# Kernel optimization log

Hardware: AMD Instinct MI355X
Metric: run time of the kernel (lower is better)

The kernel has to match this reference:

```python
import jax, jax.numpy as jnp
import numpy as np

T, B, V, E = 256, 128, 256, 512
NN = (1024, 1024)  # num_nodes per LSTM layer


def setup_inputs() -> dict:
    key = jax.random.key(0)
    ks = jax.random.split(key, 8)
    inputs = jax.random.normal(ks[0], (T, B, V), jnp.float32)
    emb = jax.random.normal(ks[1], (V, E), jnp.float32) * np.float32(np.sqrt(1.0 / V))
    w0 = jax.random.normal(ks[2], (E + NN[0], 4 * NN[0]), jnp.float32) * np.float32(np.sqrt(1.0 / (E + NN[0])))
    b0 = jnp.zeros((4 * NN[0],), jnp.float32)
    w1 = jax.random.normal(ks[3], (NN[0] + NN[1], 4 * NN[1]), jnp.float32) * np.float32(np.sqrt(1.0 / (NN[0] + NN[1])))
    b1 = jnp.zeros((4 * NN[1],), jnp.float32)
    out_w = jax.random.normal(ks[4], (NN[1], V), jnp.float32) * np.float32(np.sqrt(1.0 / NN[1]))
    out_b = jnp.zeros((V,), jnp.float32)
    return {"inputs": inputs, "embedding_matrix": emb,
            "lstm_w0": w0, "lstm_b0": b0, "lstm_w1": w1, "lstm_b1": b1,
            "out_w": out_w, "out_b": out_b}


def reference(inputs, embedding_matrix, lstm_w0, lstm_b0, lstm_w1, lstm_b1, out_w, out_b):
    Tn, Bn, _ = inputs.shape
    # _embed: (stacked one-hot) @ embedding_matrix -> [T, B, E]
    embs = jnp.einsum('tbv,ve->tbe', inputs, embedding_matrix)
    ws = (lstm_w0, lstm_w1)
    bs = (lstm_b0, lstm_b1)
    init_states = tuple((jnp.zeros((Bn, n), embs.dtype), jnp.zeros((Bn, n), embs.dtype)) for n in NN)

    def step(states, emb):
        out = emb
        new_states = []
        for i in range(len(NN)):
            h, c = states[i]
            n = NN[i]
            # concat([dropout(inp), h]) @ W + b ; dropout_keep_prob = 1.0 -> identity
            lin = jnp.concatenate([out, h], axis=1) @ ws[i] + bs[i]
            f = jax.nn.sigmoid(lin[:, :n])
            ig = jax.nn.sigmoid(lin[:, n:2 * n])
            o = jax.nn.sigmoid(lin[:, 2 * n:3 * n])
            g = jnp.tanh(lin[:, 3 * n:])
            c = f * c + ig * g
            h = o * jnp.tanh(c)
            out = h
            new_states.append((h, c))
        return tuple(new_states), out

    _, rnn_outputs = jax.lax.scan(step, init_states, embs)  # [T, B, NN[-1]]
    # output module: concat over time (axis 0) then single dense layer
    hs = rnn_outputs.reshape(Tn * Bn, NN[-1])
    logits = hs @ out_w + out_b  # [T*B, V]
    return logits
```

## Files before the change

### kernel.cpp

```cpp
#include <hip/hip_runtime.h>
#include <hip/hip_bf16.h>
#include <cstdint>
#include <cstddef>

#define T_STEPS 256
#define BATCH   128
#define VOCAB   256
#define EDIM    512
#define NH      1024
#define GDIM    4096
#define NST0    40
#define NST1    64

typedef __attribute__((ext_vector_type(8))) short short8;
typedef __attribute__((ext_vector_type(4))) float floatx4;

__device__ __forceinline__ float sigmoidf_(float x) { return 1.0f / (1.0f + __expf(-x)); }
__device__ __forceinline__ float tanhf_(float x)    { return 1.0f - 2.0f / (__expf(2.0f * x) + 1.0f); }

typedef __attribute__((address_space(1))) const unsigned int guint;
typedef __attribute__((address_space(3))) unsigned int luint;
__device__ __forceinline__ void load_lds16(const void* g, void* l) {
    __builtin_amdgcn_global_load_lds((guint*)g, (luint*)l, 16, 0, 0);
}

#define BM 128
#define BN 128
#define BK 16
__global__ __launch_bounds__(256) void sgemm_f32(
    const float* __restrict__ A, const float* __restrict__ B,
    float* __restrict__ C, int M, int N, int K)
{
    __shared__ float As[BK][BM + 4];
    __shared__ float Bs[BK][BN + 4];
    const int tid = threadIdx.x;
    const int tr = tid >> 4, tc = tid & 15;
    const int bm = blockIdx.y, bn = blockIdx.x;
    const float* Ab = A + (size_t)bm * BM * K;
    float acc[8][8];
    #pragma unroll
    for (int i = 0; i < 8; ++i)
        #pragma unroll
        for (int j = 0; j < 8; ++j) acc[i][j] = 0.f;
    for (int k0 = 0; k0 < K; k0 += BK) {
        #pragma unroll
        for (int l = 0; l < 2; ++l) {
            int idx = tid + l * 256;
            int row = idx >> 2, c4 = idx & 3;
            float4 v = *(const float4*)(Ab + (size_t)row * K + k0 + c4 * 4);
            As[c4 * 4 + 0][row] = v.x; As[c4 * 4 + 1][row] = v.y;
            As[c4 * 4 + 2][row] = v.z; As[c4 * 4 + 3][row] = v.w;
        }
        #pragma unroll
        for (int l = 0; l < 2; ++l) {
            int idx = tid + l * 256;
            int row = idx >> 5, c4 = idx & 31;
            *(float4*)&Bs[row][c4 * 4] = *(const float4*)(B + (size_t)(k0 + row) * N + bn * BN + c4 * 4);
        }
        __syncthreads();
        #pragma unroll
        for (int kk = 0; kk < BK; ++kk) {
            float4 a0 = *(const float4*)&As[kk][tr * 8];
            float4 a1 = *(const float4*)&As[kk][tr * 8 + 4];
            float4 b0 = *(const float4*)&Bs[kk][tc * 8];
            float4 b1 = *(const float4*)&Bs[kk][tc * 8 + 4];
            float av[8] = {a0.x, a0.y, a0.z, a0.w, a1.x, a1.y, a1.z, a1.w};
            float bv[8] = {b0.x, b0.y, b0.z, b0.w, b1.x, b1.y, b1.z, b1.w};
            #pragma unroll
            for (int i = 0; i < 8; ++i)
                #pragma unroll
                for (int j = 0; j < 8; ++j) acc[i][j] += av[i] * bv[j];
        }
        __syncthreads();
    }
    #pragma unroll
    for (int i = 0; i < 8; ++i) {
        size_t row = (size_t)bm * BM + tr * 8 + i;
        #pragma unroll
        for (int j = 0; j < 8; j += 4) {
            int col = bn * BN + tc * 8 + j;
            *(float4*)(C + row * N + col) =
                make_float4(acc[i][j], acc[i][j+1], acc[i][j+2], acc[i][j+3]);
        }
    }
}

__global__ __launch_bounds__(256) void transpose_to_bf16(
    const float* __restrict__ src, __hip_bfloat16* __restrict__ dst, int R, int C)
{
    __shared__ float t[32][33];
    int x = blockIdx.x * 32 + threadIdx.x;
    #pragma unroll
    for (int i = 0; i < 4; ++i) {
        int y = blockIdx.y * 32 + threadIdx.y + i * 8;
        t[threadIdx.y + i * 8][threadIdx.x] = src[(size_t)y * C + x];
    }
    __syncthreads();
    int x2 = blockIdx.y * 32 + threadIdx.x;
    #pragma unroll
    for (int i = 0; i < 4; ++i) {
        int y2 = blockIdx.x * 32 + threadIdx.y + i * 8;
        dst[(size_t)y2 * R + x2] = __float2bfloat16(t[threadIdx.x][threadIdx.y + i * 8]);
    }
}

__global__ __launch_bounds__(256) void pack_w2(
    const float* __restrict__ src, __hip_bfloat16* __restrict__ dst,
    int koff, int NSTEPS)
{
    __shared__ float t[64][33];
    const int tid = threadIdx.x;
    const int xt = blockIdx.x;
    const int kt = blockIdx.y;
    {
        int yl = tid >> 3;
        int x0 = (tid & 7) * 8;
        const float* p = src + (size_t)(kt * 32 + yl) * GDIM + xt * 64 + x0;
        float4 v0 = *(const float4*)p;
        float4 v1 = *(const float4*)(p + 4);
        t[x0 + 0][yl] = v0.x; t[x0 + 1][yl] = v0.y; t[x0 + 2][yl] = v0.z; t[x0 + 3][yl] = v0.w;
        t[x0 + 4][yl] = v1.x; t[x0 + 5][yl] = v1.y; t[x0 + 6][yl] = v1.z; t[x0 + 7][yl] = v1.w;
    }
    __syncthreads();
    {
        int ll = tid >> 2;
        int quad = tid & 3;
        int lincol = xt * 64 + ll;
        int g = lincol >> 10, n = lincol & 1023;
        int j = n >> 3, c = n & 7;
        int tt = g >> 1;
        int l16 = (g & 1) * 8 + c;
        int s = (koff >> 5) + kt;
        __hip_bfloat16 o[8];
        #pragma unroll
        for (int jj = 0; jj < 8; ++jj)
            o[jj] = __float2bfloat16(t[ll][quad * 8 + jj]);
        size_t off = ((((size_t)j * NSTEPS + s) * 2 + tt) * 64 + (size_t)quad * 16 + l16) * 8;
        *(uint4*)(dst + off) = *(const uint4*)o;
    }
}

__global__ __launch_bounds__(256) void convert_to_bf16(
    const float* __restrict__ src, __hip_bfloat16* __restrict__ dst, size_t n4)
{
    size_t i = (size_t)blockIdx.x * 256 + threadIdx.x;
    if (i < n4) {
        float4 v = *(const float4*)(src + i * 4);
        __hip_bfloat16 o[4] = {__float2bfloat16(v.x), __float2bfloat16(v.y),
                               __float2bfloat16(v.z), __float2bfloat16(v.w)};
        *(uint2*)(dst + i * 4) = *(uint2*)o;
    }
}

#define GKP 40
__global__ __launch_bounds__(256) void gemm_bt(
    const __hip_bfloat16* __restrict__ A, const __hip_bfloat16* __restrict__ Bt,
    const float* __restrict__ bias, float* __restrict__ C, int M, int N, int K)
{
    __shared__ __hip_bfloat16 As[128 * GKP];
    __shared__ __hip_bfloat16 Bs[128 * GKP];
    const int tid = threadIdx.x;
    const int wave = tid >> 6, lane = tid & 63;
    const int quad = lane >> 4, l16 = lane & 15;
    const int wm = (wave >> 1) * 64, wn = (wave & 1) * 64;
    const size_t Arow0 = (size_t)blockIdx.y * 128;
    const size_t Brow0 = (size_t)blockIdx.x * 128;
    floatx4 acc[4][4];
    #pragma unroll
    for (int i = 0; i < 4; ++i)
        #pragma unroll
        for (int j = 0; j < 4; ++j) acc[i][j] = (floatx4)0.f;

    for (int k0 = 0; k0 < K; k0 += 32) {
        #pragma unroll
        for (int l = 0; l < 2; ++l) {
            int idx = tid + l * 256;
            int row = idx >> 2, seg = idx & 3;
            *(uint4*)(As + row * GKP + seg * 8) =
                *(const uint4*)(A + (Arow0 + row) * K + k0 + seg * 8);
            *(uint4*)(Bs + row * GKP + seg * 8) =
                *(const uint4*)(Bt + (Brow0 + row) * K + k0 + seg * 8);
        }
        __syncthreads();
        short8 af[4], bf[4];
        #pragma unroll
        for (int i = 0; i < 4; ++i)
            af[i] = *(const short8*)(As + (wm + i * 16 + l16) * GKP + quad * 8);
        #pragma unroll
        for (int j = 0; j < 4; ++j)
            bf[j] = *(const short8*)(Bs + (wn + j * 16 + l16) * GKP + quad * 8);
        #pragma unroll
        for (int i = 0; i < 4; ++i)
            #pragma unroll
            for (int j = 0; j < 4; ++j)
                acc[i][j] = __builtin_amdgcn_mfma_f32_16x16x32_bf16(af[i], bf[j], acc[i][j], 0, 0, 0);
        __syncthreads();
    }
    #pragma unroll
    for (int i = 0; i < 4; ++i)
        #pragma unroll
        for (int j = 0; j < 4; ++j) {
            int col = (int)Brow0 + wn + j * 16 + l16;
            float bv = bias ? bias[col] : 0.f;
            #pragma unroll
            for (int r = 0; r < 4; ++r) {
                size_t row = Arow0 + wm + i * 16 + quad * 4 + r;
                C[row * N + col] = acc[i][j][r] + bv;
            }
        }
}

template<int NC, int W>
__device__ __forceinline__ void seg_run(
    const __hip_bfloat16* __restrict__ pA,
    const __hip_bfloat16* Wlds, int lane,
    floatx4& acc0, floatx4& acc1)
{
    constexpr int D = (NC < 3) ? NC : 3;
    short8 af[3][8];
    #pragma unroll
    for (int c = 0; c < D; ++c)
        #pragma unroll
        for (int ss = 0; ss < 8; ++ss)
            af[c][ss] = *(const short8*)(pA + (size_t)c * 256 + ss * 32);
    #pragma unroll
    for (int c = 0; c < NC; ++c) {
        #pragma unroll
        for (int ss = 0; ss < 8; ++ss) {
            const int s = (W + c) * 8 + ss;
            short8 bf0 = *(const short8*)&Wlds[s * 1024 + lane * 8];
            short8 bf1 = *(const short8*)&Wlds[s * 1024 + 512 + lane * 8];
            acc0 = __builtin_amdgcn_mfma_f32_16x16x32_bf16(af[c % 3][ss], bf0, acc0, 0, 0, 0);
            acc1 = __builtin_amdgcn_mfma_f32_16x16x32_bf16(af[c % 3][ss], bf1, acc1, 0, 0, 0);
        }
        if (c + 3 < NC) {
            #pragma unroll
            for (int ss = 0; ss < 8; ++ss)
                af[(c + 3) % 3][ss] = *(const short8*)(pA + (size_t)(c + 3) * 256 + ss * 32);
        }
    }
}

__global__ __launch_bounds__(512) void lstm_diag(
    const __hip_bfloat16* __restrict__ inbf,
    const __hip_bfloat16* __restrict__ Wpack0,
    const __hip_bfloat16* __restrict__ Wpack1,
    const float* __restrict__ b0, const float* __restrict__ b1,
    __hip_bfloat16* __restrict__ h0_cur,
    const __hip_bfloat16* __restrict__ h0_prev,
    float* __restrict__ c0, float* __restrict__ c1,
    __hip_bfloat16* __restrict__ H1all,
    int d)
{
    const int bid = blockIdx.x;
    const int layer = (bid >> 3) & 1;
    const int j = ((bid >> 4) << 3) | (bid & 7);
    if (layer == 0 && d >= T_STEPS) return;
    if (layer == 1 && d == 0) return;

    __shared__ __attribute__((aligned(16))) __hip_bfloat16 Wlds[65536];

    const int tid = threadIdx.x;
    const int wave = tid >> 6, lane = tid & 63;
    const int quad = lane >> 4, l16 = lane & 15;

    const __hip_bfloat16 *A0, *A1;
    int A0stride;
    const float* bb; float* cst; __hip_bfloat16* hout;
    bool first;
    if (layer == 0) {
        first = (d == 0);
        bb = b0; cst = c0;
        A0 = inbf + (size_t)d * (BATCH * VOCAB); A0stride = VOCAB;
        A1 = h0_prev;
        hout = h0_cur;
        const __hip_bfloat16* Wp = Wpack0 + (size_t)j * (NST0 * 1024);
        #pragma unroll
        for (int it = 0; it < 10; ++it)
            load_lds16(Wp + it * 4096 + tid * 8, Wlds + it * 4096 + tid * 8);
    } else {
        first = (d == 1);
        bb = b1; cst = c1;
        A0 = h0_prev; A0stride = NH;
        A1 = (d >= 2) ? (H1all + (size_t)(d - 2) * (BATCH * NH)) : h0_prev;
        hout = H1all + (size_t)(d - 1) * (BATCH * NH);
        const __hip_bfloat16* Wp = Wpack1 + (size_t)j * (NST1 * 1024);
        #pragma unroll
        for (int it = 0; it < 16; ++it)
            load_lds16(Wp + it * 4096 + tid * 8, Wlds + it * 4096 + tid * 8);
    }

    const int row = wave * 16 + l16;
    const __hip_bfloat16* pA0 = A0 + (size_t)row * A0stride + quad * 8;
    const __hip_bfloat16* pA1 = A1 + (size_t)row * NH + quad * 8;

    const int cc = j * 8 + (l16 & 7);
    float bv0 = bb[((l16 < 8) ? 0 : 1) * NH + cc];
    float bv1 = bb[((l16 < 8) ? 2 : 3) * NH + cc];
    float cold[4];
    {
        const int bbase = 16 * wave + quad * 4;
        #pragma unroll
        for (int r = 0; r < 4; ++r)
            cold[r] = first ? 0.f : cst[(size_t)(bbase + r) * NH + cc];
    }
    floatx4 acc0 = {bv0, bv0, bv0, bv0};
    floatx4 acc1 = {bv1, bv1, bv1, bv1};

    __syncthreads();
    if (layer == 0) {
        seg_run<1, 0>(pA0, Wlds, lane, acc0, acc1);
        if (!first) seg_run<4, 1>(pA1, Wlds, lane, acc0, acc1);
    } else {
        if (first) {
            seg_run<4, 0>(pA0, Wlds, lane, acc0, acc1);
        } else {
            seg_run<4, 4>(pA1, Wlds, lane, acc0, acc1);
            seg_run<4, 0>(pA0, Wlds, lane, acc0, acc1);
        }
    }

    #pragma unroll
    for (int r = 0; r < 4; ++r) {
        float a0 = acc0[r], a1 = acc1[r];
        float p0 = __shfl_xor(a0, 8, 64);
        float p1 = __shfl_xor(a1, 8, 64);
        if (l16 < 8) {
            int b = 16 * wave + quad * 4 + r;
            float f  = sigmoidf_(a0);
            float ig = sigmoidf_(p0);
            float oo = sigmoidf_(a1);
            float gg = tanhf_(p1);
            size_t idx = (size_t)b * NH + cc;
            float cn = f * cold[r] + ig * gg;
            float hn = oo * tanhf_(cn);
            cst[idx] = cn;
            hout[idx] = __float2bfloat16(hn);
        }
    }
}

__device__ __forceinline__ void spin_all_ge(const uint32_t* ep, uint32_t target,
                                            int lane, int wave) {
    asm volatile("" ::: "memory");
    if (wave == 0) {
        for (;;) {
            uint32_t a = __hip_atomic_load(&ep[lane], __ATOMIC_RELAXED, __HIP_MEMORY_SCOPE_AGENT);
            uint32_t b = __hip_atomic_load(&ep[lane + 64], __ATOMIC_RELAXED, __HIP_MEMORY_SCOPE_AGENT);
            if (__all(a >= target && b >= target)) break;
            __builtin_amdgcn_s_sleep(1);
        }
    }
    __builtin_amdgcn_s_barrier();
    asm volatile("" ::: "memory");
}

__device__ __forceinline__ void arrive_ep(uint32_t* slot, uint32_t val) {
    __syncthreads();
    asm volatile("" ::: "memory");
    if (threadIdx.x == 0)
        __hip_atomic_store(slot, val, __ATOMIC_RELAXED, __HIP_MEMORY_SCOPE_AGENT);
}

__global__ void zero_bar(uint32_t* p) { p[threadIdx.x] = 0; }

__device__ __forceinline__ void epilogue_store(
    floatx4 acc0, floatx4 acc1, float* creg, bool first,
    int wave, int quad, int l16, int cc8base,
    __hip_bfloat16* __restrict__ hout)
{
    #pragma unroll
    for (int r = 0; r < 4; ++r) {
        float a0 = acc0[r], a1 = acc1[r];
        float p0 = __shfl_xor(a0, 8, 64);
        float p1 = __shfl_xor(a1, 8, 64);
        float f  = sigmoidf_(a0);
        float ig = sigmoidf_(p0);
        float oo = sigmoidf_(a1);
        float gg = tanhf_(p1);
        float cn = f * (first ? 0.f : creg[r]) + ig * gg;
        if (l16 < 8) creg[r] = cn;
        float hn = oo * tanhf_(cn);
        union { __hip_bfloat16 h; unsigned short u; } cv;
        cv.h = __float2bfloat16(hn);
        unsigned int v1 = (unsigned int)cv.u |
                          (__shfl_xor((unsigned int)cv.u, 1, 64) << 16);
        unsigned int v2 = __shfl_xor(v1, 2, 64);
        unsigned long long p8 = (unsigned long long)v1 |
                                ((unsigned long long)v2 << 32);
        if (l16 == 0 || l16 == 4) {
            int b = 16 * wave + quad * 4 + r;
            __hip_atomic_store((unsigned long long*)&hout[(size_t)b * NH + cc8base + l16],
                               p8, __ATOMIC_RELAXED, __HIP_MEMORY_SCOPE_AGENT);
        }
    }
}

__global__ __launch_bounds__(512) void lstm_persist6(
    const __hip_bfloat16* __restrict__ inbf,
    const __hip_bfloat16* __restrict__ Wpack0,
    const __hip_bfloat16* __restrict__ Wpack1,
    const float* __restrict__ b0, const float* __restrict__ b1,
    __hip_bfloat16* __restrict__ H0all,
    __hip_bfloat16* __restrict__ H1all,
    uint32_t* __restrict__ bar)
{
    __shared__ __attribute__((aligned(16))) __hip_bfloat16 Wlds[65536];

    const int bid = blockIdx.x;
    const int layer = (bid >> 3) & 1;
    const int j = ((bid >> 4) << 3) | (bid & 7);
    const int tid = threadIdx.x;
    const int wave = tid >> 6, lane = tid & 63;
    const int quad = lane >> 4, l16 = lane & 15;

    uint32_t* ep0 = bar;
    uint32_t* ep1 = bar + 128;

    if (layer == 0) {
        const __hip_bfloat16* Wp = Wpack0 + (size_t)j * (NST0 * 1024);
        #pragma unroll
        for (int it = 0; it < 10; ++it)
            load_lds16(Wp + it * 4096 + tid * 8, Wlds + it * 4096 + tid * 8);
    } else {
        const __hip_bfloat16* Wp = Wpack1 + (size_t)j * (NST1 * 1024);
        #pragma unroll
        for (int it = 0; it < 16; ++it)
            load_lds16(Wp + it * 4096 + tid * 8, Wlds + it * 4096 + tid * 8);
    }
    __syncthreads();

    const int cc = j * 8 + (l16 & 7);
    const float* bb = layer ? b1 : b0;
    const float bv0 = bb[((l16 < 8) ? 0 : 1) * NH + cc];
    const float bv1 = bb[((l16 < 8) ? 2 : 3) * NH + cc];
    const int row = wave * 16 + l16;
    float creg[4] = {0.f, 0.f, 0.f, 0.f};

    if (layer == 0) {
        for (int d = 0; d < T_STEPS; ++d) {
            const bool first = (d == 0);
            const __hip_bfloat16* pX =
                inbf + (size_t)d * (BATCH * VOCAB) + (size_t)row * VOCAB + quad * 8;
            __hip_bfloat16* hout = H0all + (size_t)d * (BATCH * NH);
            floatx4 acc0 = {bv0, bv0, bv0, bv0};
            floatx4 acc1 = {bv1, bv1, bv1, bv1};
            seg_run<1, 0>(pX, Wlds, lane, acc0, acc1);
            if (!first) {
                spin_all_ge(ep0, (uint32_t)d, lane, wave);
                const __hip_bfloat16* pH0 =
                    H0all + (size_t)(d - 1) * (BATCH * NH) + (size_t)row * NH + quad * 8;
                seg_run<4, 1>(pH0, Wlds, lane, acc0, acc1);
            }
            epilogue_store(acc0, acc1, creg, first, wave, quad, l16, j * 8, hout);
            arrive_ep(&ep0[j], (uint32_t)(d + 1));
        }
    } else {
        for (int d = 1; d <= T_STEPS; ++d) {
            const bool first = (d == 1);
            __hip_bfloat16* hout = H1all + (size_t)(d - 1) * (BATCH * NH);
            floatx4 acc0 = {bv0, bv0, bv0, bv0};
            floatx4 acc1 = {bv1, bv1, bv1, bv1};
            if (!first) {
                spin_all_ge(ep1, (uint32_t)(d - 1), lane, wave);
                const __hip_bfloat16* pH1 =
                    H1all + (size_t)(d - 2) * (BATCH * NH) + (size_t)row * NH + quad * 8;
                seg_run<4, 4>(pH1, Wlds, lane, acc0, acc1);
            }
            spin_all_ge(ep0, (uint32_t)d, lane, wave);
            const __hip_bfloat16* pH0 =
                H0all + (size_t)(d - 1) * (BATCH * NH) + (size_t)row * NH + quad * 8;
            seg_run<4, 0>(pH0, Wlds, lane, acc0, acc1);
            epilogue_store(acc0, acc1, creg, first, wave, quad, l16, j * 8, hout);
            arrive_ep(&ep1[j], (uint32_t)d);
        }
    }
}

extern "C" void kernel_launch(void* const* d_in, const int* in_sizes, int n_in,
                              void* d_out, int out_size, void* d_ws, size_t ws_size,
                              hipStream_t stream)
{
    const float* inputs = (const float*)d_in[0];
    const float* emb    = (const float*)d_in[1];
    const float* w0     = (const float*)d_in[2];
    const float* b0     = (const float*)d_in[3];
    const float* w1     = (const float*)d_in[4];
    const float* b1     = (const float*)d_in[5];
    const float* outw   = (const float*)d_in[6];
    const float* outb   = (const float*)d_in[7];
    float* out = (float*)d_out;

    char* ws = (char*)d_ws;
    size_t off = 0;
    auto take = [&](size_t bytes) { char* p = ws + off; off += (bytes + 255) & ~(size_t)255; return p; };
    float* Wcomb = (float*)take((size_t)VOCAB * GDIM * 4);
    __hip_bfloat16* Wpack0 = (__hip_bfloat16*)take((size_t)128 * NST0 * 1024 * 2);
    __hip_bfloat16* Wpack1 = (__hip_bfloat16*)take((size_t)128 * NST1 * 1024 * 2);
    __hip_bfloat16* outwt  = (__hip_bfloat16*)take((size_t)NH * VOCAB * 2);
    __hip_bfloat16* inbf   = (__hip_bfloat16*)take((size_t)T_STEPS * BATCH * VOCAB * 2);
    __hip_bfloat16* h0pp0  = (__hip_bfloat16*)take((size_t)BATCH * NH * 2);
    __hip_bfloat16* h0pp1  = (__hip_bfloat16*)take((size_t)BATCH * NH * 2);
    float* c0 = (float*)take((size_t)BATCH * NH * 4);
    float* c1 = (float*)take((size_t)BATCH * NH * 4);
    uint32_t* bar = (uint32_t*)take(1024);
    __hip_bfloat16* H1all  = (__hip_bfloat16*)take((size_t)T_STEPS * BATCH * NH * 2);
    __hip_bfloat16* H0all  = (__hip_bfloat16*)take((size_t)T_STEPS * BATCH * NH * 2);
    const bool ws_ok = (off <= ws_size);

    sgemm_f32<<<dim3(GDIM / BN, VOCAB / BM), 256, 0, stream>>>(
        emb, w0, Wcomb, VOCAB, GDIM, EDIM);
    pack_w2<<<dim3(64, VOCAB / 32), 256, 0, stream>>>(Wcomb, Wpack0, 0, NST0);
    pack_w2<<<dim3(64, NH / 32), 256, 0, stream>>>(w0 + (size_t)EDIM * GDIM, Wpack0, VOCAB, NST0);
    pack_w2<<<dim3(64, NH / 32), 256, 0, stream>>>(w1, Wpack1, 0, NST1);
    pack_w2<<<dim3(64, NH / 32), 256, 0, stream>>>(w1 + (size_t)NH * GDIM, Wpack1, NH, NST1);
    transpose_to_bf16<<<dim3(VOCAB / 32, NH / 32), dim3(32, 8), 0, stream>>>(
        outw, outwt, NH, VOCAB);
    {
        size_t n4 = (size_t)T_STEPS * BATCH * VOCAB / 4;
        convert_to_bf16<<<(int)((n4 + 255) / 256), 256, 0, stream>>>(inputs, inbf, n4);
    }
    zero_bar<<<1, 256, 0, stream>>>(bar);

    bool done = false;
    if (ws_ok) {
        void* args[] = { (void*)&inbf, (void*)&Wpack0, (void*)&Wpack1,
                         (void*)&b0, (void*)&b1,
                         (void*)&H0all, (void*)&H1all, (void*)&bar };
        hipError_t ce = hipLaunchCooperativeKernel(lstm_persist6, dim3(256), dim3(512),
                                                   args, 0u, stream);
        done = (ce == hipSuccess);
    }
    if (!done) {
        for (int d = 0; d <= T_STEPS; ++d) {
            __hip_bfloat16* hcur = (d & 1) ? h0pp1 : h0pp0;
            __hip_bfloat16* hprev = (d & 1) ? h0pp0 : h0pp1;
            lstm_diag<<<256, 512, 0, stream>>>(
                inbf, Wpack0, Wpack1, b0, b1, hcur, hprev, c0, c1, H1all, d);
        }
    }

    gemm_bt<<<dim3(VOCAB / 128, (T_STEPS * BATCH) / 128), 256, 0, stream>>>(
        H1all, outwt, outb, out, T_STEPS * BATCH, VOCAB, NH);
}
```

Before: 4.793 ms.

## Hold LSTM weights in registers and split K across waves with LDS reduction

The persistent LSTM kernel no longer keeps its weight slice in LDS. Each wave now holds its share of the K dimension as MFMA B-fragments in registers, computes all 128 batch rows for that K-slice, and the per-wave partial sums are reduced through LDS before the gate epilogue. Every wave now spins on the barrier flags itself instead of wave 0 spinning and then calling s_barrier, and launch bounds ask for two blocks per CU. The aim is to remove repeated LDS weight reads and shorten the dependency chain per step. In exchange it adds an LDS reduction and a __syncthreads each step, and it puts heavy pressure on registers from the 8x2 accumulators plus the weight fragments.

```diff
diff --git a/kernel.cpp b/kernel.cpp
--- a/kernel.cpp
+++ b/kernel.cpp
@@ -340,18 +340,14 @@
     }
 }
 
-__device__ __forceinline__ void spin_all_ge(const uint32_t* ep, uint32_t target,
-                                            int lane, int wave) {
+__device__ __forceinline__ void spin_wave(const uint32_t* ep, uint32_t target, int lane) {
     asm volatile("" ::: "memory");
-    if (wave == 0) {
-        for (;;) {
-            uint32_t a = __hip_atomic_load(&ep[lane], __ATOMIC_RELAXED, __HIP_MEMORY_SCOPE_AGENT);
-            uint32_t b = __hip_atomic_load(&ep[lane + 64], __ATOMIC_RELAXED, __HIP_MEMORY_SCOPE_AGENT);
-            if (__all(a >= target && b >= target)) break;
-            __builtin_amdgcn_s_sleep(1);
-        }
-    }
-    __builtin_amdgcn_s_barrier();
+    for (;;) {
+        uint32_t a = __hip_atomic_load(&ep[lane], __ATOMIC_RELAXED, __HIP_MEMORY_SCOPE_AGENT);
+        uint32_t b = __hip_atomic_load(&ep[lane + 64], __ATOMIC_RELAXED, __HIP_MEMORY_SCOPE_AGENT);
+        if (__all(a >= target && b >= target)) break;
+        __builtin_amdgcn_s_sleep(1);
+    }
     asm volatile("" ::: "memory");
 }
 
@@ -396,7 +392,7 @@
     }
 }
 
-__global__ __launch_bounds__(512) void lstm_persist6(
+__global__ __launch_bounds__(512, 2) void lstm_persist7(
     const __hip_bfloat16* __restrict__ inbf,
     const __hip_bfloat16* __restrict__ Wpack0,
     const __hip_bfloat16* __restrict__ Wpack1,
@@ -405,75 +401,155 @@
     __hip_bfloat16* __restrict__ H1all,
     uint32_t* __restrict__ bar)
 {
-    __shared__ __attribute__((aligned(16))) __hip_bfloat16 Wlds[65536];
+    __shared__ __attribute__((aligned(16))) float red[32768];
 
     const int bid = blockIdx.x;
     const int layer = (bid >> 3) & 1;
     const int j = ((bid >> 4) << 3) | (bid & 7);
     const int tid = threadIdx.x;
-    const int wave = tid >> 6, lane = tid & 63;
+    const int wv = tid >> 6, lane = tid & 63;
     const int quad = lane >> 4, l16 = lane & 15;
 
     uint32_t* ep0 = bar;
     uint32_t* ep1 = bar + 128;
 
+    short8 breg[8][2];
     if (layer == 0) {
         const __hip_bfloat16* Wp = Wpack0 + (size_t)j * (NST0 * 1024);
         #pragma unroll
-        for (int it = 0; it < 10; ++it)
-            load_lds16(Wp + it * 4096 + tid * 8, Wlds + it * 4096 + tid * 8);
+        for (int t = 0; t < 2; ++t)
+            breg[0][t] = *(const short8*)(Wp + ((size_t)wv * 2 + t) * 512 + lane * 8);
+        #pragma unroll
+        for (int i = 0; i < 4; ++i) {
+            const int ks = 8 + 4 * wv + i;
+            #pragma unroll
+            for (int t = 0; t < 2; ++t)
+                breg[1 + i][t] = *(const short8*)(Wp + ((size_t)ks * 2 + t) * 512 + lane * 8);
+        }
+        #pragma unroll
+        for (int i = 5; i < 8; ++i) {
+            breg[i][0] = breg[0][0];
+            breg[i][1] = breg[0][1];
+        }
     } else {
         const __hip_bfloat16* Wp = Wpack1 + (size_t)j * (NST1 * 1024);
         #pragma unroll
-        for (int it = 0; it < 16; ++it)
-            load_lds16(Wp + it * 4096 + tid * 8, Wlds + it * 4096 + tid * 8);
-    }
-    __syncthreads();
+        for (int i = 0; i < 4; ++i) {
+            const int ks1 = 32 + 4 * wv + i;
+            const int ks0 = 4 * wv + i;
+            #pragma unroll
+            for (int t = 0; t < 2; ++t) {
+                breg[i][t]     = *(const short8*)(Wp + ((size_t)ks1 * 2 + t) * 512 + lane * 8);
+                breg[4 + i][t] = *(const short8*)(Wp + ((size_t)ks0 * 2 + t) * 512 + lane * 8);
+            }
+        }
+    }
 
     const int cc = j * 8 + (l16 & 7);
     const float* bb = layer ? b1 : b0;
     const float bv0 = bb[((l16 < 8) ? 0 : 1) * NH + cc];
     const float bv1 = bb[((l16 < 8) ? 2 : 3) * NH + cc];
-    const int row = wave * 16 + l16;
     float creg[4] = {0.f, 0.f, 0.f, 0.f};
 
-    if (layer == 0) {
-        for (int d = 0; d < T_STEPS; ++d) {
-            const bool first = (d == 0);
-            const __hip_bfloat16* pX =
-                inbf + (size_t)d * (BATCH * VOCAB) + (size_t)row * VOCAB + quad * 8;
-            __hip_bfloat16* hout = H0all + (size_t)d * (BATCH * NH);
-            floatx4 acc0 = {bv0, bv0, bv0, bv0};
-            floatx4 acc1 = {bv1, bv1, bv1, bv1};
-            seg_run<1, 0>(pX, Wlds, lane, acc0, acc1);
+    const int hcol = 4 * wv * 32 + quad * 8;
+    const int xcol = wv * 32 + quad * 8;
+
+    const int dlo = layer ? 1 : 0;
+    const int dhi = layer ? T_STEPS : (T_STEPS - 1);
+
+    for (int d = dlo; d <= dhi; ++d) {
+        const bool first = (d == dlo);
+        floatx4 acc[8][2];
+        #pragma unroll
+        for (int m = 0; m < 8; ++m) {
+            acc[m][0] = (floatx4)0.f;
+            acc[m][1] = (floatx4)0.f;
+        }
+
+        __hip_bfloat16* hout;
+        if (layer == 0) {
+            const __hip_bfloat16* pX = inbf + (size_t)d * (BATCH * VOCAB);
+            {
+                short8 af[8];
+                #pragma unroll
+                for (int m = 0; m < 8; ++m)
+                    af[m] = *(const short8*)(pX + (size_t)(m * 16 + l16) * VOCAB + xcol);
+                #pragma unroll
+                for (int m = 0; m < 8; ++m) {
+                    acc[m][0] = __builtin_amdgcn_mfma_f32_16x16x32_bf16(af[m], breg[0][0], acc[m][0], 0, 0, 0);
+                    acc[m][1] = __builtin_amdgcn_mfma_f32_16x16x32_bf16(af[m], breg[0][1], acc[m][1], 0, 0, 0);
+                }
+            }
             if (!first) {
-                spin_all_ge(ep0, (uint32_t)d, lane, wave);
-                const __hip_bfloat16* pH0 =
-                    H0all + (size_t)(d - 1) * (BATCH * NH) + (size_t)row * NH + quad * 8;
-                seg_run<4, 1>(pH0, Wlds, lane, acc0, acc1);
+                spin_wave(ep0, (uint32_t)d, lane);
+                const __hip_bfloat16* pH0 = H0all + (size_t)(d - 1) * (BATCH * NH);
+                #pragma unroll
+                for (int i = 0; i < 4; ++i) {
+                    short8 af[8];
+                    #pragma unroll
+                    for (int m = 0; m < 8; ++m)
+                        af[m] = *(const short8*)(pH0 + (size_t)(m * 16 + l16) * NH + hcol + i * 32);
+                    #pragma unroll
+                    for (int m = 0; m < 8; ++m) {
+                        acc[m][0] = __builtin_amdgcn_mfma_f32_16x16x32_bf16(af[m], breg[1 + i][0], acc[m][0], 0, 0, 0);
+                        acc[m][1] = __builtin_amdgcn_mfma_f32_16x16x32_bf16(af[m], breg[1 + i][1], acc[m][1], 0, 0, 0);
+                    }
+                }
             }
-            epilogue_store(acc0, acc1, creg, first, wave, quad, l16, j * 8, hout);
-            arrive_ep(&ep0[j], (uint32_t)(d + 1));
-        }
-    } else {
-        for (int d = 1; d <= T_STEPS; ++d) {
-            const bool first = (d == 1);
-            __hip_bfloat16* hout = H1all + (size_t)(d - 1) * (BATCH * NH);
-            floatx4 acc0 = {bv0, bv0, bv0, bv0};
-            floatx4 acc1 = {bv1, bv1, bv1, bv1};
+            hout = H0all + (size_t)d * (BATCH * NH);
+        } else {
             if (!first) {
-                spin_all_ge(ep1, (uint32_t)(d - 1), lane, wave);
-                const __hip_bfloat16* pH1 =
-                    H1all + (size_t)(d - 2) * (BATCH * NH) + (size_t)row * NH + quad * 8;
-                seg_run<4, 4>(pH1, Wlds, lane, acc0, acc1);
+                spin_wave(ep1, (uint32_t)(d - 1), lane);
+                const __hip_bfloat16* pH1 = H1all + (size_t)(d - 2) * (BATCH * NH);
+                #pragma unroll
+                for (int i = 0; i < 4; ++i) {
+                    short8 af[8];
+                    #pragma unroll
+                    for (int m = 0; m < 8; ++m)
+                        af[m] = *(const short8*)(pH1 + (size_t)(m * 16 + l16) * NH + hcol + i * 32);
+                    #pragma unroll
+                    for (int m = 0; m < 8; ++m) {
+                        acc[m][0] = __builtin_amdgcn_mfma_f32_16x16x32_bf16(af[m], breg[i][0], acc[m][0], 0, 0, 0);
+                        acc[m][1] = __builtin_amdgcn_mfma_f32_16x16x32_bf16(af[m], breg[i][1], acc[m][1], 0, 0, 0);
+                    }
+                }
             }
-            spin_all_ge(ep0, (uint32_t)d, lane, wave);
-            const __hip_bfloat16* pH0 =
-                H0all + (size_t)(d - 1) * (BATCH * NH) + (size_t)row * NH + quad * 8;
-            seg_run<4, 0>(pH0, Wlds, lane, acc0, acc1);
-            epilogue_store(acc0, acc1, creg, first, wave, quad, l16, j * 8, hout);
-            arrive_ep(&ep1[j], (uint32_t)d);
-        }
+            spin_wave(ep0, (uint32_t)d, lane);
+            const __hip_bfloat16* pH0 = H0all + (size_t)(d - 1) * (BATCH * NH);
+            #pragma unroll
+            for (int i = 0; i < 4; ++i) {
+                short8 af[8];
+                #pragma unroll
+                for (int m = 0; m < 8; ++m)
+                    af[m] = *(const short8*)(pH0 + (size_t)(m * 16 + l16) * NH + hcol + i * 32);
+                #pragma unroll
+                for (int m = 0; m < 8; ++m) {
+                    acc[m][0] = __builtin_amdgcn_mfma_f32_16x16x32_bf16(af[m], breg[4 + i][0], acc[m][0], 0, 0, 0);
+                    acc[m][1] = __builtin_amdgcn_mfma_f32_16x16x32_bf16(af[m], breg[4 + i][1], acc[m][1], 0, 0, 0);
+                }
+            }
+            hout = H1all + (size_t)(d - 1) * (BATCH * NH);
+        }
+
+        #pragma unroll
+        for (int m = 0; m < 8; ++m) {
+            *(floatx4*)&red[((((wv * 2 + 0) * 8 + m) * 64) + l16 * 4 + quad) * 4] = acc[m][0];
+            *(floatx4*)&red[((((wv * 2 + 1) * 8 + m) * 64) + l16 * 4 + quad) * 4] = acc[m][1];
+        }
+        __syncthreads();
+
+        floatx4 s0 = (floatx4)0.f, s1 = (floatx4)0.f;
+        #pragma unroll
+        for (int w = 0; w < 8; ++w) {
+            s0 += *(const floatx4*)&red[((((w * 2 + 0) * 8 + wv) * 64) + l16 * 4 + quad) * 4];
+            s1 += *(const floatx4*)&red[((((w * 2 + 1) * 8 + wv) * 64) + l16 * 4 + quad) * 4];
+        }
+        s0 += bv0;
+        s1 += bv1;
+
+        epilogue_store(s0, s1, creg, first, wv, quad, l16, j * 8, hout);
+
+        arrive_ep(layer ? &ep1[j] : &ep0[j], (uint32_t)(layer ? d : d + 1));
     }
 }
 
@@ -527,7 +603,7 @@
         void* args[] = { (void*)&inbf, (void*)&Wpack0, (void*)&Wpack1,
                          (void*)&b0, (void*)&b1,
                          (void*)&H0all, (void*)&H1all, (void*)&bar };
-        hipError_t ce = hipLaunchCooperativeKernel(lstm_persist6, dim3(256), dim3(512),
+        hipError_t ce = hipLaunchCooperativeKernel(lstm_persist7, dim3(256), dim3(512),
                                                    args, 0u, stream);
         done = (ce == hipSuccess);
     }
```

After: 5.419 ms. 13.1% more time.
